# Kernel optimization log

Hardware: AMD Instinct MI355X
Metric: run time of the kernel (lower is better)

## Reference

```python
import jax, jax.numpy as jnp
import numpy as np

T, B, E, H = 512, 32, 512, 2048

def setup_inputs() -> dict:
    key = jax.random.key(0)
    k1, k2, k3 = jax.random.split(key, 3)
    sent = jax.random.normal(k1, (T, B, E), dtype=jnp.float32)
    lengths = jax.random.randint(k2, (B,), 1, T + 1)  # unused by the math (pack is never applied)
    # Linear(E, 3H) params (PyTorch default-ish init scale)
    W = jax.random.normal(k3, (3 * H, E), dtype=jnp.float32) * (1.0 / np.sqrt(E))
    b = jnp.zeros((3 * H,), dtype=jnp.float32)
    return {"sent": sent, "lengths": lengths, "W": W, "b": b}

def reference(sent, lengths, W, b):
    # sent: (T, B, E) time-major. Single QRNN layer, window=1, output_gate=True, zoneout=0.
    Y = jnp.einsum('tbe,he->tbh', sent, W) + b          # (T, B, 3H)
    Z, F, O = jnp.split(Y, 3, axis=-1)
    Z = jnp.tanh(Z)
    F = jax.nn.sigmoid(F)
    O = jax.nn.sigmoid(O)

    # forget-mult recurrence: c_t = f_t * z_t + (1 - f_t) * c_{t-1}, c_0 = 0
    def step(c, zf):
        z, f = zf
        c = f * z + (1.0 - f) * c
        return c, c
    c0 = jnp.zeros_like(Z[0])                            # (B, H)
    _, C = jax.lax.scan(step, c0, (Z, F))                # (T, B, H)

    Hseq = O * C                                         # QRNN output (T, B, H)
    embeds = jnp.max(Hseq, axis=0)                       # torch.max(sent_output, 0)[0] -> (B, H)
    return embeds
```

## Files before the change

kernel.cpp:

```cpp
#include <hip/hip_runtime.h>
#include <stdint.h>

#define TT 512
#define BB 32
#define EE 512
#define HH 2048

typedef __attribute__((ext_vector_type(8))) short short8;
typedef __attribute__((ext_vector_type(4))) float f32x4;

#define XROW 528
#define XBUF (16 * XROW)

#define BAR_VM0() asm volatile("s_waitcnt vmcnt(0) lgkmcnt(0)\n\ts_barrier" ::: "memory")

static __device__ __forceinline__ float fast_exp(float x) {
    return __builtin_amdgcn_exp2f(x * 1.44269504f);
}
static __device__ __forceinline__ float fast_rcp(float x) {
    return __builtin_amdgcn_rcpf(x);
}

static __device__ __forceinline__ unsigned cvtpk_bf16(float lo, float hi) {
    unsigned r;
    asm("v_cvt_pk_bf16_f32 %0, %1, %2" : "=v"(r) : "v"(lo), "v"(hi));
    return r;
}

static __device__ __forceinline__ void load_lds16(const unsigned short* g, unsigned short* l) {
    __builtin_amdgcn_global_load_lds(
        (const __attribute__((address_space(1))) unsigned int*)(uintptr_t)g,
        (__attribute__((address_space(3))) unsigned int*)(uintptr_t)l,
        16, 0, 0);
}

__global__ void convert_inputs(const float* __restrict__ X,
                               const float* __restrict__ W,
                               unsigned short* __restrict__ Xb,
                               unsigned short* __restrict__ Wb) {
    const int nX = TT * BB * EE;
    const int nT = (nX + 3 * HH * EE) / 8;
    const int stride = gridDim.x * blockDim.x;
    for (int g = blockIdx.x * blockDim.x + threadIdx.x; g < nT; g += stride) {
        int i = g * 8;
        const float* src;
        unsigned short* dst;
        int j;
        if (i < nX) { src = X; dst = Xb; j = i; }
        else        { src = W; dst = Wb; j = i - nX; }
        float4 v0 = *(const float4*)(src + j);
        float4 v1 = *(const float4*)(src + j + 4);
        union { short8 s; unsigned u[4]; } o;
        o.u[0] = cvtpk_bf16(v0.x, v0.y);
        o.u[1] = cvtpk_bf16(v0.z, v0.w);
        o.u[2] = cvtpk_bf16(v1.x, v1.y);
        o.u[3] = cvtpk_bf16(v1.z, v1.w);
        *(short8*)(dst + j) = o.s;
    }
}

__launch_bounds__(256, 2)
__global__ void qrnn_fused(const unsigned short* __restrict__ Xb,
                           const unsigned short* __restrict__ Wb,
                           const float* __restrict__ bias,
                           float* __restrict__ out)
{
    __shared__ unsigned short xlds[2 * XBUF];
    __shared__ float rawx[2][2][64][12];
    __shared__ float actx[2][2][64][12];

    const int tid  = threadIdx.x;
    const int wv   = tid >> 6;
    const int lane = tid & 63;
    const int q    = lane >> 4;
    const int c    = lane & 15;
    const int hi   = wv >> 1;
    const int s    = wv & 1;

    const int id   = blockIdx.x;
    const int xcd  = id & 7;
    const int slot = id >> 3;
    const int b    = xcd * 4 + (slot >> 6);
    const int hgrp = slot & 63;
    const int h    = hgrp * 32 + hi * 16 + c;

    short8 wz[8], wf[8], wo[8];
    {
        const unsigned short* wzr = Wb + (size_t)h * EE            + s * 256;
        const unsigned short* wfr = Wb + (size_t)(HH + h) * EE     + s * 256;
        const unsigned short* wor = Wb + (size_t)(2 * HH + h) * EE + s * 256;
#pragma unroll
        for (int k = 0; k < 8; ++k) {
            int e0 = k * 32 + q * 8;
            wz[k] = *(const short8*)(wzr + e0);
            wf[k] = *(const short8*)(wfr + e0);
            wo[k] = *(const short8*)(wor + e0);
        }
    }
#pragma unroll
    for (int k = 0; k < 8; ++k) {
        asm volatile("" : "+a"(wz[k]), "+a"(wf[k]), "+a"(wo[k]));
    }

    const float b0 = bias[h];
    const float b1 = bias[HH + h];
    const float b2 = bias[2 * HH + h];

    float carry = 0.0f;
    float vmax  = -1e30f;

    const unsigned short* g0 = Xb + ((size_t)(wv * 4) * BB + b) * EE + lane * 8;
    unsigned short* l0 = &xlds[(wv * 4) * XROW];

    auto stage = [&](int n, int slt) {
        const unsigned short* g = g0 + (size_t)n * (16 * BB * EE);
        unsigned short* l = l0 + slt * XBUF;
#pragma unroll
        for (int i = 0; i < 4; ++i)
            load_lds16(g + (size_t)i * (BB * EE), l + i * XROW);
    };

    auto do_act = [&](int n, f32x4 sz, f32x4 sf, f32x4 so) {
        float* e = &actx[n & 1][hi][lane][0];
#pragma unroll
        for (int r = 0; r < 4; ++r) {
            float zz = sz[r] + b0;
            float ff = sf[r] + b1;
            float oo = so[r] + b2;
            float e2 = fast_exp(2.0f * zz);
            float z  = 1.0f - 2.0f * fast_rcp(e2 + 1.0f);
            float f  = fast_rcp(1.0f + fast_exp(-ff));
            float o  = fast_rcp(1.0f + fast_exp(-oo));
            e[r]     = f * z;
            e[4 + r] = 1.0f - f;
            e[8 + r] = o;
        }
    };

    auto do_scan = [&](int n) {
        const float* e = &actx[n & 1][hi][lane][0];
        float aa[4], mm[4], oo[4];
#pragma unroll
        for (int r = 0; r < 4; ++r) {
            aa[r] = e[r];
            mm[r] = e[4 + r];
            oo[r] = e[8 + r];
        }

        float A = aa[0], M = mm[0];
#pragma unroll
        for (int r = 1; r < 4; ++r) { A = aa[r] + mm[r] * A; M = mm[r] * M; }

        float Ap = __shfl_up(A, 16, 64), Mp = __shfl_up(M, 16, 64);
        if (q >= 1) { A = A + M * Ap; M = M * Mp; }
        Ap = __shfl_up(A, 32, 64); Mp = __shfl_up(M, 32, 64);
        if (q >= 2) { A = A + M * Ap; M = M * Mp; }
        float Ae = __shfl_up(A, 16, 64), Me = __shfl_up(M, 16, 64);
        if (q == 0) { Ae = 0.0f; Me = 1.0f; }
        float cc = Ae + Me * carry;

#pragma unroll
        for (int r = 0; r < 4; ++r) {
            cc = aa[r] + mm[r] * cc;
            vmax = fmaxf(vmax, oo[r] * cc);
        }

        float cend = A + M * carry;
        carry = __shfl(cend, 48 + c, 64);
    };

    stage(0, 0);
    BAR_VM0();

    f32x4 prevz, prevf, prevo;

    for (int ch = 0; ch < 32; ++ch) {
        const int buf = ch & 1;
        if (ch < 31) stage(ch + 1, buf ^ 1);

        const unsigned short* Abase = &xlds[buf * XBUF + c * XROW + s * 256 + q * 8];
        short8 a[8];
#pragma unroll
        for (int k = 0; k < 8; ++k)
            a[k] = *(const short8*)(Abase + k * 32);

        f32x4 az = {0.f, 0.f, 0.f, 0.f};
        f32x4 af = {0.f, 0.f, 0.f, 0.f};
        f32x4 ao = {0.f, 0.f, 0.f, 0.f};
#pragma unroll
        for (int k = 0; k < 8; ++k) {
            az = __builtin_amdgcn_mfma_f32_16x16x32_bf16(a[k], wz[k], az, 0, 0, 0);
            af = __builtin_amdgcn_mfma_f32_16x16x32_bf16(a[k], wf[k], af, 0, 0, 0);
            ao = __builtin_amdgcn_mfma_f32_16x16x32_bf16(a[k], wo[k], ao, 0, 0, 0);
        }

        if (s == 0) {
            float* e = &rawx[ch & 1][hi][lane][0];
            *(f32x4*)(e)     = az;
            *(f32x4*)(e + 4) = af;
            *(f32x4*)(e + 8) = ao;

            if (ch > 1) do_scan(ch - 2);
        } else {
            if (ch > 0) {
                const float* e = &rawx[(ch - 1) & 1][hi][lane][0];
                f32x4 sz = prevz + *(const f32x4*)(e);
                f32x4 sf = prevf + *(const f32x4*)(e + 4);
                f32x4 so = prevo + *(const f32x4*)(e + 8);
                do_act(ch - 1, sz, sf, so);
            }
            prevz = az; prevf = af; prevo = ao;
        }

        BAR_VM0();
    }

    if (s == 1) {
        const float* e = &rawx[31 & 1][hi][lane][0];
        f32x4 sz = prevz + *(const f32x4*)(e);
        f32x4 sf = prevf + *(const f32x4*)(e + 4);
        f32x4 so = prevo + *(const f32x4*)(e + 8);
        do_act(31, sz, sf, so);
    }
    BAR_VM0();

    if (s == 0) {
        do_scan(30);
        do_scan(31);

        vmax = fmaxf(vmax, __shfl_xor(vmax, 16, 64));
        vmax = fmaxf(vmax, __shfl_xor(vmax, 32, 64));
        if (q == 0) out[(size_t)b * HH + h] = vmax;
    }
}

extern "C" void kernel_launch(void* const* d_in, const int* in_sizes, int n_in,
                              void* d_out, int out_size, void* d_ws, size_t ws_size,
                              hipStream_t stream) {
    const float* sent = (const float*)d_in[0];
    const float* W    = (const float*)d_in[2];
    const float* bias = (const float*)d_in[3];
    float* out        = (float*)d_out;

    const int nX = TT * BB * EE;
    const int nW = 3 * HH * EE;
    unsigned short* Xb = (unsigned short*)d_ws;
    unsigned short* Wb = Xb + nX;

    convert_inputs<<<2048, 256, 0, stream>>>(sent, W, Xb, Wb);

    dim3 grid(2048);
    qrnn_fused<<<grid, 256, 0, stream>>>(Xb, Wb, bias, out);
}
```

Baseline: 238.3 us.

## Transpose X to batch-major and load MFMA operands directly from global

The conversion kernel now writes X in (B,T,E) order, one row per wavefront, so each block's timesteps sit in contiguous memory. The fused kernel drops the LDS staging buffer and global_load_lds, and reads A fragments straight from global (L2-resident) memory. It processes 32 timesteps per chunk with half as many barriers, and the bias is folded into the accumulator init on one K-half. This trades LDS traffic and barrier count for exposed global-load latency, since there is no explicit prefetch and the barrier no longer waits on vmcnt.

```diff
diff --git a/kernel.cpp b/kernel.cpp
--- a/kernel.cpp
+++ b/kernel.cpp
@@ -9,10 +9,9 @@
 typedef __attribute__((ext_vector_type(8))) short short8;
 typedef __attribute__((ext_vector_type(4))) float f32x4;
 
-#define XROW 528
-#define XBUF (16 * XROW)
-
-#define BAR_VM0() asm volatile("s_waitcnt vmcnt(0) lgkmcnt(0)\n\ts_barrier" ::: "memory")
+#define ESTR 28
+
+#define BAR_LGKM() asm volatile("s_waitcnt lgkmcnt(0)\n\ts_barrier" ::: "memory")
 
 static __device__ __forceinline__ float fast_exp(float x) {
     return __builtin_amdgcn_exp2f(x * 1.44269504f);
@@ -27,35 +26,34 @@
     return r;
 }
 
-static __device__ __forceinline__ void load_lds16(const unsigned short* g, unsigned short* l) {
-    __builtin_amdgcn_global_load_lds(
-        (const __attribute__((address_space(1))) unsigned int*)(uintptr_t)g,
-        (__attribute__((address_space(3))) unsigned int*)(uintptr_t)l,
-        16, 0, 0);
-}
-
 __global__ void convert_inputs(const float* __restrict__ X,
                                const float* __restrict__ W,
                                unsigned short* __restrict__ Xb,
                                unsigned short* __restrict__ Wb) {
-    const int nX = TT * BB * EE;
-    const int nT = (nX + 3 * HH * EE) / 8;
-    const int stride = gridDim.x * blockDim.x;
-    for (int g = blockIdx.x * blockDim.x + threadIdx.x; g < nT; g += stride) {
-        int i = g * 8;
+    const int xRows = TT * BB;
+    const int totRows = xRows + 3 * HH;
+    const int lane = threadIdx.x & 63;
+    const int nw = (gridDim.x * blockDim.x) >> 6;
+    for (int r = (blockIdx.x * blockDim.x + threadIdx.x) >> 6; r < totRows; r += nw) {
         const float* src;
         unsigned short* dst;
-        int j;
-        if (i < nX) { src = X; dst = Xb; j = i; }
-        else        { src = W; dst = Wb; j = i - nX; }
-        float4 v0 = *(const float4*)(src + j);
-        float4 v1 = *(const float4*)(src + j + 4);
+        if (r < xRows) {
+            int t = r >> 5, b = r & 31;
+            src = X + (size_t)r * EE;
+            dst = Xb + ((size_t)b * TT + t) * EE;
+        } else {
+            int wr = r - xRows;
+            src = W + (size_t)wr * EE;
+            dst = Wb + (size_t)wr * EE;
+        }
+        float4 v0 = *(const float4*)(src + lane * 8);
+        float4 v1 = *(const float4*)(src + lane * 8 + 4);
         union { short8 s; unsigned u[4]; } o;
         o.u[0] = cvtpk_bf16(v0.x, v0.y);
         o.u[1] = cvtpk_bf16(v0.z, v0.w);
         o.u[2] = cvtpk_bf16(v1.x, v1.y);
         o.u[3] = cvtpk_bf16(v1.z, v1.w);
-        *(short8*)(dst + j) = o.s;
+        *(short8*)(dst + lane * 8) = o.s;
     }
 }
 
@@ -65,9 +63,8 @@
                            const float* __restrict__ bias,
                            float* __restrict__ out)
 {
-    __shared__ unsigned short xlds[2 * XBUF];
-    __shared__ float rawx[2][2][64][12];
-    __shared__ float actx[2][2][64][12];
+    __shared__ float rawx[2][2][64][ESTR];
+    __shared__ float actx[2][2][64][ESTR];
 
     const int tid  = threadIdx.x;
     const int wv   = tid >> 6;
@@ -102,50 +99,34 @@
         asm volatile("" : "+a"(wz[k]), "+a"(wf[k]), "+a"(wo[k]));
     }
 
-    const float b0 = bias[h];
-    const float b1 = bias[HH + h];
-    const float b2 = bias[2 * HH + h];
+    const float b0 = (s == 0) ? bias[h]          : 0.0f;
+    const float b1 = (s == 0) ? bias[HH + h]     : 0.0f;
+    const float b2 = (s == 0) ? bias[2 * HH + h] : 0.0f;
 
     float carry = 0.0f;
     float vmax  = -1e30f;
 
-    const unsigned short* g0 = Xb + ((size_t)(wv * 4) * BB + b) * EE + lane * 8;
-    unsigned short* l0 = &xlds[(wv * 4) * XROW];
-
-    auto stage = [&](int n, int slt) {
-        const unsigned short* g = g0 + (size_t)n * (16 * BB * EE);
-        unsigned short* l = l0 + slt * XBUF;
-#pragma unroll
-        for (int i = 0; i < 4; ++i)
-            load_lds16(g + (size_t)i * (BB * EE), l + i * XROW);
+    const unsigned short* Xp = Xb + (size_t)b * TT * EE;
+    const int aoff = s * 256 + q * 8;
+
+    auto burst = [&](int t0, f32x4& az, f32x4& af, f32x4& ao) {
+        const unsigned short* Ab = Xp + (size_t)(t0 + c) * EE + aoff;
+        short8 a[8];
+#pragma unroll
+        for (int k = 0; k < 8; ++k)
+            a[k] = *(const short8*)(Ab + k * 32);
+#pragma unroll
+        for (int k = 0; k < 8; ++k) {
+            az = __builtin_amdgcn_mfma_f32_16x16x32_bf16(a[k], wz[k], az, 0, 0, 0);
+            af = __builtin_amdgcn_mfma_f32_16x16x32_bf16(a[k], wf[k], af, 0, 0, 0);
+            ao = __builtin_amdgcn_mfma_f32_16x16x32_bf16(a[k], wo[k], ao, 0, 0, 0);
+        }
     };
 
-    auto do_act = [&](int n, f32x4 sz, f32x4 sf, f32x4 so) {
-        float* e = &actx[n & 1][hi][lane][0];
-#pragma unroll
-        for (int r = 0; r < 4; ++r) {
-            float zz = sz[r] + b0;
-            float ff = sf[r] + b1;
-            float oo = so[r] + b2;
-            float e2 = fast_exp(2.0f * zz);
-            float z  = 1.0f - 2.0f * fast_rcp(e2 + 1.0f);
-            float f  = fast_rcp(1.0f + fast_exp(-ff));
-            float o  = fast_rcp(1.0f + fast_exp(-oo));
-            e[r]     = f * z;
-            e[4 + r] = 1.0f - f;
-            e[8 + r] = o;
-        }
-    };
-
-    auto do_scan = [&](int n) {
-        const float* e = &actx[n & 1][hi][lane][0];
+    auto scan16 = [&](f32x4 aav, f32x4 mmv, f32x4 oov) {
         float aa[4], mm[4], oo[4];
 #pragma unroll
-        for (int r = 0; r < 4; ++r) {
-            aa[r] = e[r];
-            mm[r] = e[4 + r];
-            oo[r] = e[8 + r];
-        }
+        for (int r = 0; r < 4; ++r) { aa[r] = aav[r]; mm[r] = mmv[r]; oo[r] = oov[r]; }
 
         float A = aa[0], M = mm[0];
 #pragma unroll
@@ -169,64 +150,91 @@
         carry = __shfl(cend, 48 + c, 64);
     };
 
-    stage(0, 0);
-    BAR_VM0();
-
-    f32x4 prevz, prevf, prevo;
-
-    for (int ch = 0; ch < 32; ++ch) {
-        const int buf = ch & 1;
-        if (ch < 31) stage(ch + 1, buf ^ 1);
-
-        const unsigned short* Abase = &xlds[buf * XBUF + c * XROW + s * 256 + q * 8];
-        short8 a[8];
-#pragma unroll
-        for (int k = 0; k < 8; ++k)
-            a[k] = *(const short8*)(Abase + k * 32);
-
-        f32x4 az = {0.f, 0.f, 0.f, 0.f};
-        f32x4 af = {0.f, 0.f, 0.f, 0.f};
-        f32x4 ao = {0.f, 0.f, 0.f, 0.f};
-#pragma unroll
-        for (int k = 0; k < 8; ++k) {
-            az = __builtin_amdgcn_mfma_f32_16x16x32_bf16(a[k], wz[k], az, 0, 0, 0);
-            af = __builtin_amdgcn_mfma_f32_16x16x32_bf16(a[k], wf[k], af, 0, 0, 0);
-            ao = __builtin_amdgcn_mfma_f32_16x16x32_bf16(a[k], wo[k], ao, 0, 0, 0);
-        }
+    auto act4 = [&](f32x4 sz, f32x4 sf, f32x4 so, f32x4& aav, f32x4& mmv, f32x4& oov) {
+#pragma unroll
+        for (int r = 0; r < 4; ++r) {
+            float e2 = fast_exp(2.0f * sz[r]);
+            float z  = 1.0f - 2.0f * fast_rcp(e2 + 1.0f);
+            float f  = fast_rcp(1.0f + fast_exp(-sf[r]));
+            float o  = fast_rcp(1.0f + fast_exp(-so[r]));
+            aav[r] = f * z;
+            mmv[r] = 1.0f - f;
+            oov[r] = o;
+        }
+    };
+
+    f32x4 ownzA, ownfA, ownoA, ownzB, ownfB, ownoB;
+
+    for (int ch = 0; ch < 16; ++ch) {
+        f32x4 azA = {b0, b0, b0, b0}, afA = {b1, b1, b1, b1}, aoA = {b2, b2, b2, b2};
+        f32x4 azB = {b0, b0, b0, b0}, afB = {b1, b1, b1, b1}, aoB = {b2, b2, b2, b2};
+        burst(ch * 32,      azA, afA, aoA);
+        burst(ch * 32 + 16, azB, afB, aoB);
 
         if (s == 0) {
-            float* e = &rawx[ch & 1][hi][lane][0];
-            *(f32x4*)(e)     = az;
-            *(f32x4*)(e + 4) = af;
-            *(f32x4*)(e + 8) = ao;
-
-            if (ch > 1) do_scan(ch - 2);
+            float* w = &rawx[ch & 1][hi][lane][0];
+            *(f32x4*)(w)      = azA;  *(f32x4*)(w + 4)  = azB;
+            *(f32x4*)(w + 8)  = afA;  *(f32x4*)(w + 12) = afB;
+            *(f32x4*)(w + 16) = aoA;  *(f32x4*)(w + 20) = aoB;
+
+            if (ch > 1) {
+                const float* e = &actx[ch & 1][hi][lane][0];
+                scan16(*(const f32x4*)(e),     *(const f32x4*)(e + 8),  *(const f32x4*)(e + 16));
+                scan16(*(const f32x4*)(e + 4), *(const f32x4*)(e + 12), *(const f32x4*)(e + 20));
+            }
         } else {
             if (ch > 0) {
-                const float* e = &rawx[(ch - 1) & 1][hi][lane][0];
-                f32x4 sz = prevz + *(const f32x4*)(e);
-                f32x4 sf = prevf + *(const f32x4*)(e + 4);
-                f32x4 so = prevo + *(const f32x4*)(e + 8);
-                do_act(ch - 1, sz, sf, so);
+                const float* rr = &rawx[(ch - 1) & 1][hi][lane][0];
+                f32x4 szA = ownzA + *(const f32x4*)(rr);
+                f32x4 szB = ownzB + *(const f32x4*)(rr + 4);
+                f32x4 sfA = ownfA + *(const f32x4*)(rr + 8);
+                f32x4 sfB = ownfB + *(const f32x4*)(rr + 12);
+                f32x4 soA = ownoA + *(const f32x4*)(rr + 16);
+                f32x4 soB = ownoB + *(const f32x4*)(rr + 20);
+                f32x4 aaA, mmA, ooA, aaB, mmB, ooB;
+                act4(szA, sfA, soA, aaA, mmA, ooA);
+                act4(szB, sfB, soB, aaB, mmB, ooB);
+                float* e = &actx[(ch - 1) & 1][hi][lane][0];
+                *(f32x4*)(e)      = aaA;  *(f32x4*)(e + 4)  = aaB;
+                *(f32x4*)(e + 8)  = mmA;  *(f32x4*)(e + 12) = mmB;
+                *(f32x4*)(e + 16) = ooA;  *(f32x4*)(e + 20) = ooB;
             }
-            prevz = az; prevf = af; prevo = ao;
-        }
-
-        BAR_VM0();
+            ownzA = azA; ownfA = afA; ownoA = aoA;
+            ownzB = azB; ownfB = afB; ownoB = aoB;
+        }
+
+        BAR_LGKM();
     }
 
     if (s == 1) {
-        const float* e = &rawx[31 & 1][hi][lane][0];
-        f32x4 sz = prevz + *(const f32x4*)(e);
-        f32x4 sf = prevf + *(const f32x4*)(e + 4);
-        f32x4 so = prevo + *(const f32x4*)(e + 8);
-        do_act(31, sz, sf, so);
-    }
-    BAR_VM0();
+        const float* rr = &rawx[15 & 1][hi][lane][0];
+        f32x4 szA = ownzA + *(const f32x4*)(rr);
+        f32x4 szB = ownzB + *(const f32x4*)(rr + 4);
+        f32x4 sfA = ownfA + *(const f32x4*)(rr + 8);
+        f32x4 sfB = ownfB + *(const f32x4*)(rr + 12);
+        f32x4 soA = ownoA + *(const f32x4*)(rr + 16);
+        f32x4 soB = ownoB + *(const f32x4*)(rr + 20);
+        f32x4 aaA, mmA, ooA, aaB, mmB, ooB;
+        act4(szA, sfA, soA, aaA, mmA, ooA);
+        act4(szB, sfB, soB, aaB, mmB, ooB);
+        float* e = &actx[15 & 1][hi][lane][0];
+        *(f32x4*)(e)      = aaA;  *(f32x4*)(e + 4)  = aaB;
+        *(f32x4*)(e + 8)  = mmA;  *(f32x4*)(e + 12) = mmB;
+        *(f32x4*)(e + 16) = ooA;  *(f32x4*)(e + 20) = ooB;
+    }
+    BAR_LGKM();
 
     if (s == 0) {
-        do_scan(30);
-        do_scan(31);
+        {
+            const float* e = &actx[0][hi][lane][0];
+            scan16(*(const f32x4*)(e),     *(const f32x4*)(e + 8),  *(const f32x4*)(e + 16));
+            scan16(*(const f32x4*)(e + 4), *(const f32x4*)(e + 12), *(const f32x4*)(e + 20));
+        }
+        {
+            const float* e = &actx[1][hi][lane][0];
+            scan16(*(const f32x4*)(e),     *(const f32x4*)(e + 8),  *(const f32x4*)(e + 16));
+            scan16(*(const f32x4*)(e + 4), *(const f32x4*)(e + 12), *(const f32x4*)(e + 20));
+        }
 
         vmax = fmaxf(vmax, __shfl_xor(vmax, 16, 64));
         vmax = fmaxf(vmax, __shfl_xor(vmax, 32, 64));
@@ -243,11 +251,10 @@
     float* out        = (float*)d_out;
 
     const int nX = TT * BB * EE;
-    const int nW = 3 * HH * EE;
     unsigned short* Xb = (unsigned short*)d_ws;
     unsigned short* Wb = Xb + nX;
 
-    convert_inputs<<<2048, 256, 0, stream>>>(sent, W, Xb, Wb);
+    convert_inputs<<<1024, 256, 0, stream>>>(sent, W, Xb, Wb);
 
     dim3 grid(2048);
     qrnn_fused<<<grid, 256, 0, stream>>>(Xb, Wb, bias, out);
```

After: 369.4 us. +55.0%, slower.
